# Kernel tuning notes

Hardware: AMD Instinct MI355X
Metric: run time of the kernel (lower is better)

## Reference

```python
import jax, jax.numpy as jnp
import numpy as np

# RVQECell configuration (matches init_kwargs)
I_SZ, W_SZ, STAGES, ORDER, DEGREE = 6, 12, 3, 2, 2
BIAS = float(np.pi / 2)
ANC = ORDER - 1                      # ancillas_for_order(order) = order - 1
N = I_SZ + W_SZ + ANC                # 19 qubits
B = 32
INOUT = list(range(I_SZ))            # lanes 0..5
WORK = list(range(I_SZ, I_SZ + W_SZ))  # lanes 6..17
C_CTRL = I_SZ + W_SZ - 1             # controls per neuron = 17


def setup_inputs() -> dict:
    key = jax.random.key(0)
    ks = jax.random.split(key, 9)
    s = 0.1  # small init keeps neuron angles in a well-conditioned range
    psi = jax.random.normal(ks[0], (B, 2 ** N), jnp.float32)
    psi = psi / jnp.linalg.norm(psi, axis=1, keepdims=True)  # normalized kets
    return {
        "batch": psi,
        "w_in1": jax.random.normal(ks[1], (W_SZ, C_CTRL), jnp.float32) * s,
        "w_in2": jax.random.normal(ks[2], (W_SZ, C_CTRL, C_CTRL), jnp.float32) * s,
        "w_u": jax.random.normal(ks[3], (STAGES, W_SZ), jnp.float32) * s,
        "w_k1": jax.random.normal(ks[4], (STAGES, W_SZ, C_CTRL), jnp.float32) * s,
        "w_k2": jax.random.normal(ks[5], (STAGES, W_SZ, C_CTRL, C_CTRL), jnp.float32) * s,
        "w_out1": jax.random.normal(ks[6], (I_SZ, C_CTRL), jnp.float32) * s,
        "w_out2": jax.random.normal(ks[7], (I_SZ, C_CTRL, C_CTRL), jnp.float32) * s,
        "inputs": jax.random.randint(ks[8], (B, I_SZ), 0, 2, dtype=jnp.int32),
    }


def _rot_y(state, lane, alpha):
    # real rotation [[cos a, -sin a], [sin a, cos a]] on qubit `lane`.
    ax = lane + 1  # +1 for batch axis; state shape [B] + [2]*N
    c, s = jnp.cos(alpha), jnp.sin(alpha)
    p0 = jax.lax.index_in_dim(state, 0, ax, keepdims=True)
    p1 = jax.lax.index_in_dim(state, 1, ax, keepdims=True)
    return jnp.concatenate([c * p0 - s * p1, s * p0 + c * p1], axis=ax)


def _neuron(state, outlane, th1, th2):
    # Fast (deterministic RUS) quantum neuron of given ORDER/DEGREE:
    # per control-basis-branch rotation of `outlane` by alpha(x),
    # phi(x) = bias + sum_i th1_i x_i + sum_{i<j} th2_ij x_i x_j (degree 2),
    # alpha = q^(order-1)(phi), q(t) = arctan(tan(t)^2), stable via arctan2.
    controls = [l for l in range(I_SZ + W_SZ) if l != outlane]
    Cn = len(controls)
    x = jnp.arange(2 ** Cn)
    shifts = jnp.arange(Cn - 1, -1, -1)
    bits = ((x[:, None] >> shifts[None, :]) & 1).astype(state.dtype)  # [2^Cn, Cn]
    phi = BIAS + bits @ th1
    if DEGREE >= 2:
        phi = phi + jnp.einsum('xi,ij,xj->x', bits, jnp.triu(th2, 1), bits)
    alpha = phi
    for _ in range(ORDER - 1):
        alpha = jnp.arctan2(jnp.sin(alpha) ** 2, jnp.cos(alpha) ** 2)
    shape = [1] + [2 if l in controls else 1 for l in range(N)]
    return _rot_y(state, outlane, alpha.reshape(shape))


def _bitflip(state_flat, inputs):
    # Vectorized batched BitFlipLayer: X on inout lane i where inputs[b,i]==1,
    # i.e. permute amplitudes by XOR of the flip mask (lane 0 most significant).
    shifts = (N - 1) - jnp.arange(I_SZ)
    f = jnp.sum(inputs.astype(jnp.int32) << shifts[None, :], axis=1)  # [B]
    idx = jnp.arange(2 ** N, dtype=jnp.int32)[None, :] ^ f[:, None]
    return jnp.take_along_axis(state_flat, idx, axis=1)


def reference(batch, w_in1, w_in2, w_u, w_k1, w_k2, w_out1, w_out2, inputs):
    psi = _bitflip(batch, inputs).reshape((B,) + (2,) * N)
    # input layer: one neuron per workspace lane
    for j, out in enumerate(WORK):
        psi = _neuron(psi, out, w_in1[j], w_in2[j])
    # kernel layer: stages x (UnitaryLayer(workspace) + neurons)
    for st in range(STAGES):
        for j, lane in enumerate(WORK):
            psi = _rot_y(psi, lane, w_u[st, j])
        for j, out in enumerate(WORK):
            psi = _neuron(psi, out, w_k1[st, j], w_k2[st, j])
    psi = _bitflip(psi.reshape(B, -1), inputs).reshape((B,) + (2,) * N)
    # output layer: one neuron per inout lane
    for j, out in enumerate(INOUT):
        psi = _neuron(psi, out, w_out1[j], w_out2[j])
    # measurement probabilities over inout lanes: marginal of |amp|^2
    probs = jnp.sum(psi ** 2, axis=tuple(range(1 + I_SZ, 1 + N))).reshape(B, -1)
    return probs, psi.reshape(B, -1)
```

## Files before the change

### kernel.cpp

```cpp
#include <hip/hip_runtime.h>
#include <math.h>


#define BIAS_F 1.57079632679489662f

typedef float v4f __attribute__((ext_vector_type(4)));

__device__ __forceinline__ float4 ntload4(const float* p) {
    v4f v = __builtin_nontemporal_load((const v4f*)p);
    return make_float4(v.x, v.y, v.z, v.w);
}
__device__ __forceinline__ void ntstore4(float* p, float4 f) {
    v4f v = {f.x, f.y, f.z, f.w};
    __builtin_nontemporal_store(v, (v4f*)p);
}

__device__ __forceinline__ int SW(int i) { return i ^ ((i >> 3) & 0x1C); }
__device__ __forceinline__ float4 ldsld4(const float* st, int i) {
    return *(const float4*)&st[SW(i)];
}
__device__ __forceinline__ void ldsst4(float* st, int i, float4 v) {
    *(float4*)&st[SW(i)] = v;
}

#define LD2(p) (*(const float2*)(p))
#define LD4(p) (*(const float4*)(p))

__device__ __forceinline__ void rot4(float4& A, float4& B, float4 e) {
    float ax = A.x, ay = A.y, az = A.z, aw = A.w;
    A.x = e.x * ax - e.y * B.x;  B.x = e.y * ax + e.x * B.x;
    A.y = e.x * ay - e.y * B.y;  B.y = e.y * ay + e.x * B.y;
    A.z = e.z * az - e.w * B.z;  B.z = e.w * az + e.z * B.z;
    A.w = e.z * aw - e.w * B.w;  B.w = e.w * aw + e.z * B.w;
}
__device__ __forceinline__ void rotq(float4& P, float c, float s) {
    float px = P.x, py = P.y;
    P.x = c * px - s * P.z;  P.z = s * px + c * P.z;
    P.y = c * py - s * P.w;  P.w = s * py + c * P.w;
}


__global__ __launch_bounds__(256) void tables_kernel(
    const float* __restrict__ w_in1, const float* __restrict__ w_in2,
    const float* __restrict__ w_k1,  const float* __restrict__ w_k2,
    const float* __restrict__ w_out1, const float* __restrict__ w_out2,
    float* __restrict__ tab)
{
    const int n = blockIdx.y;
    const int hi = blockIdx.x;
    const int tid = threadIdx.x;
    const float* th1;
    const float* th2;
    if (n < 12)      { th1 = w_in1 + n * 17;         th2 = w_in2 + n * 289; }
    else if (n < 48) { th1 = w_k1 + (n - 12) * 17;   th2 = w_k2 + (n - 12) * 289; }
    else             { th1 = w_out1 + (n - 48) * 17; th2 = w_out2 + (n - 48) * 289; }

    float phi_hi = BIAS_F;
    float C[8];
#pragma unroll
    for (int a = 0; a < 8; ++a) C[a] = th1[9 + a];
#pragma unroll
    for (int i = 0; i < 9; ++i) {
        if ((hi >> (8 - i)) & 1) {
            float acc = th1[i];
#pragma unroll
            for (int j = i + 1; j < 9; ++j)
                if ((hi >> (8 - j)) & 1) acc += th2[i * 17 + j];
            phi_hi += acc;
#pragma unroll
            for (int a = 0; a < 8; ++a) C[a] += th2[i * 17 + 9 + a];
        }
    }

    float bt[8];
#pragma unroll
    for (int j = 0; j < 8; ++j) bt[j] = (float)((tid >> (7 - j)) & 1);
    float phi = phi_hi;
#pragma unroll
    for (int a = 0; a < 8; ++a) {
        float acc = C[a];
#pragma unroll
        for (int b2 = a + 1; b2 < 8; ++b2) acc += bt[b2] * th2[(9 + a) * 17 + 9 + b2];
        phi += bt[a] * acc;
    }

    float sp, cp;
    sincosf(phi, &sp, &cp);
    float c2 = cp * cp, s2 = sp * sp;
    float d = c2 * c2 + s2 * s2;
    float r = rsqrtf(d);
    r = r * (1.5f - 0.5f * d * r * r);
    float2* dst = (float2*)tab + ((size_t)n * 131072 + (size_t)((hi << 8) | tid));
    *dst = make_float2(c2 * r, s2 * r);
}

template <int PA, bool NEUR>
__device__ __forceinline__ void pass_hi2(float* l0, float* l1, int t8,
    const float* tA, const float* tB, const float* tC,
    float cA, float sA, float cB, float sB, float cC, float sC)
{
    const int lowb = PA - 4;
    const int low = t8 & ((1 << lowb) - 1);
    const int high = t8 >> lowb;
    const int i0 = (high << (PA + 1)) | (low << 2);
    const int x0 = (high << (PA - 1)) | (low << 1);
    const int oa = 1 << PA, ob = oa >> 1, oc = oa >> 2;
    const int dhi = oa >> 2, dlo = oa >> 3;
    float4 ea00, ea01, ea10, ea11, eb00, eb01, eb10, eb11, ec00, ec01, ec10, ec11;
    if (NEUR) {
        ea00 = LD4(&tA[2 * x0]);            ea01 = LD4(&tA[2 * (x0 + dlo)]);
        ea10 = LD4(&tA[2 * (x0 + dhi)]);    ea11 = LD4(&tA[2 * (x0 + dhi + dlo)]);
        eb00 = LD4(&tB[2 * x0]);            eb01 = LD4(&tB[2 * (x0 + dlo)]);
        eb10 = LD4(&tB[2 * (x0 + dhi)]);    eb11 = LD4(&tB[2 * (x0 + dhi + dlo)]);
        ec00 = LD4(&tC[2 * x0]);            ec01 = LD4(&tC[2 * (x0 + dlo)]);
        ec10 = LD4(&tC[2 * (x0 + dhi)]);    ec11 = LD4(&tC[2 * (x0 + dhi + dlo)]);
    } else {
        ea00 = ea01 = ea10 = ea11 = make_float4(cA, sA, cA, sA);
        eb00 = eb01 = eb10 = eb11 = make_float4(cB, sB, cB, sB);
        ec00 = ec01 = ec10 = ec11 = make_float4(cC, sC, cC, sC);
    }
#pragma unroll
    for (int s = 0; s < 2; ++s) {
        float* sl = (s == 0) ? l0 : l1;
        float4 Q000 = ldsld4(sl, i0),            Q001 = ldsld4(sl, i0 + oc);
        float4 Q010 = ldsld4(sl, i0 + ob),       Q011 = ldsld4(sl, i0 + ob + oc);
        float4 Q100 = ldsld4(sl, i0 + oa),       Q101 = ldsld4(sl, i0 + oa + oc);
        float4 Q110 = ldsld4(sl, i0 + oa + ob),  Q111 = ldsld4(sl, i0 + oa + ob + oc);
        rot4(Q000, Q100, ea00); rot4(Q001, Q101, ea01);
        rot4(Q010, Q110, ea10); rot4(Q011, Q111, ea11);
        rot4(Q000, Q010, eb00); rot4(Q001, Q011, eb01);
        rot4(Q100, Q110, eb10); rot4(Q101, Q111, eb11);
        rot4(Q000, Q001, ec00); rot4(Q010, Q011, ec01);
        rot4(Q100, Q101, ec10); rot4(Q110, Q111, ec11);
        ldsst4(sl, i0, Q000);            ldsst4(sl, i0 + oc, Q001);
        ldsst4(sl, i0 + ob, Q010);       ldsst4(sl, i0 + ob + oc, Q011);
        ldsst4(sl, i0 + oa, Q100);       ldsst4(sl, i0 + oa + oc, Q101);
        ldsst4(sl, i0 + oa + ob, Q110);  ldsst4(sl, i0 + oa + ob + oc, Q111);
    }
}

template <bool NEUR>
__device__ __forceinline__ void pass_lo2(float* l0, float* l1, int t8,
    const float* tA, const float* tB, const float* tC,
    float cA, float sA, float cB, float sB, float cC, float sC)
{
    const int i0 = t8 << 5, x0 = t8 << 3;
    float4 ea0, ea1, ea2, ea3, eb0, eb1, eb2, eb3, ec0, ec1, ec2, ec3;
    if (NEUR) {
        ea0 = LD4(&tA[2 * x0]);      ea1 = LD4(&tA[2 * x0 + 4]);
        ea2 = LD4(&tA[2 * x0 + 8]);  ea3 = LD4(&tA[2 * x0 + 12]);
        eb0 = LD4(&tB[2 * x0]);      eb1 = LD4(&tB[2 * x0 + 4]);
        eb2 = LD4(&tB[2 * x0 + 8]);  eb3 = LD4(&tB[2 * x0 + 12]);
        ec0 = LD4(&tC[2 * x0]);      ec1 = LD4(&tC[2 * x0 + 4]);
        ec2 = LD4(&tC[2 * x0 + 8]);  ec3 = LD4(&tC[2 * x0 + 12]);
    } else {
        ea0 = ea1 = ea2 = ea3 = make_float4(cA, sA, cA, sA);
        eb0 = eb1 = eb2 = eb3 = make_float4(cB, sB, cB, sB);
        ec0 = ec1 = ec2 = ec3 = make_float4(cC, sC, cC, sC);
    }
#pragma unroll
    for (int s = 0; s < 2; ++s) {
        float* sl = (s == 0) ? l0 : l1;
        float4 Q0 = ldsld4(sl, i0),      Q1 = ldsld4(sl, i0 + 4);
        float4 Q2 = ldsld4(sl, i0 + 8),  Q3 = ldsld4(sl, i0 + 12);
        float4 Q4 = ldsld4(sl, i0 + 16), Q5 = ldsld4(sl, i0 + 20);
        float4 Q6 = ldsld4(sl, i0 + 24), Q7 = ldsld4(sl, i0 + 28);
        rot4(Q0, Q2, ea0); rot4(Q1, Q3, ea1); rot4(Q4, Q6, ea2); rot4(Q5, Q7, ea3);
        rot4(Q0, Q1, eb0); rot4(Q2, Q3, eb1); rot4(Q4, Q5, eb2); rot4(Q6, Q7, eb3);
        rotq(Q0, ec0.x, ec0.y); rotq(Q1, ec0.z, ec0.w);
        rotq(Q2, ec1.x, ec1.y); rotq(Q3, ec1.z, ec1.w);
        rotq(Q4, ec2.x, ec2.y); rotq(Q5, ec2.z, ec2.w);
        rotq(Q6, ec3.x, ec3.y); rotq(Q7, ec3.z, ec3.w);
        ldsst4(sl, i0, Q0);      ldsst4(sl, i0 + 4, Q1);
        ldsst4(sl, i0 + 8, Q2);  ldsst4(sl, i0 + 12, Q3);
        ldsst4(sl, i0 + 16, Q4); ldsst4(sl, i0 + 20, Q5);
        ldsst4(sl, i0 + 24, Q6); ldsst4(sl, i0 + 28, Q7);
    }
}

__global__ __launch_bounds__(256, 2) void main_kernel(
    const float* __restrict__ batch, const float* __restrict__ w_u,
    const int* __restrict__ inputs, const float* __restrict__ tab,
    float* __restrict__ psi, float* __restrict__ probs)
{
    __shared__ __align__(16) float lds[2][8192];
    const int t8 = threadIdx.x;
    const int blk = blockIdx.x;
    const int xcd = blk & 7;
    const int vt = (xcd << 3) | ((blk >> 3) & 7);
    const int pair = blk >> 6;

    if (blk == 0) {
        float4 z = make_float4(0.f, 0.f, 0.f, 0.f);
        *(float4*)&probs[t8 * 8] = z;
        *(float4*)&probs[t8 * 8 + 4] = z;
    }

    int bb[2], uu[2];
#pragma unroll
    for (int s = 0; s < 2; ++s) {
        int b = pair * 2 + s;
        int fb = 0;
#pragma unroll
        for (int i = 0; i < 6; ++i) fb |= (inputs[b * 6 + i] & 1) << (5 - i);
        bb[s] = b; uu[s] = vt ^ fb;
        const float* src = batch + ((size_t)b << 19) + ((size_t)uu[s] << 13);
#pragma unroll
        for (int k = 0; k < 8; ++k) {
            int i4 = (k * 256 + t8) * 4;
            float4 v = ntload4(&src[i4]);
            *(float4*)&lds[s][SW(i4)] = v;
        }
    }
    float* l0 = lds[0];
    float* l1 = lds[1];

    const float* tb = tab + ((size_t)vt << 12);
#define TN(j) (tb + (size_t)(j) * 262144)
#define BAR __syncthreads()
    BAR;
    pass_hi2<12, true>(l0, l1, t8, TN(0), TN(1), TN(2), 0,0,0,0,0,0);  BAR;
    pass_hi2<9,  true>(l0, l1, t8, TN(3), TN(4), TN(5), 0,0,0,0,0,0);  BAR;
    pass_hi2<6,  true>(l0, l1, t8, TN(6), TN(7), TN(8), 0,0,0,0,0,0);  BAR;
    pass_lo2<true>(l0, l1, t8, TN(9), TN(10), TN(11), 0,0,0,0,0,0);    BAR;

#pragma unroll 1
    for (int st2 = 0; st2 < 3; ++st2) {
        const float* wu = w_u + st2 * 12;
        float c0, s0, c1, s1, c2, s2;
        sincosf(wu[0], &s0, &c0); sincosf(wu[1], &s1, &c1); sincosf(wu[2], &s2, &c2);
        pass_hi2<12, false>(l0, l1, t8, 0,0,0, c0,s0, c1,s1, c2,s2);   BAR;
        sincosf(wu[3], &s0, &c0); sincosf(wu[4], &s1, &c1); sincosf(wu[5], &s2, &c2);
        pass_hi2<9, false>(l0, l1, t8, 0,0,0, c0,s0, c1,s1, c2,s2);    BAR;
        sincosf(wu[6], &s0, &c0); sincosf(wu[7], &s1, &c1); sincosf(wu[8], &s2, &c2);
        pass_hi2<6, false>(l0, l1, t8, 0,0,0, c0,s0, c1,s1, c2,s2);    BAR;
        sincosf(wu[9], &s0, &c0); sincosf(wu[10], &s1, &c1); sincosf(wu[11], &s2, &c2);
        pass_lo2<false>(l0, l1, t8, 0,0,0, c0,s0, c1,s1, c2,s2);       BAR;

        const int nb = 12 + st2 * 12;
        pass_hi2<12, true>(l0, l1, t8, TN(nb+0), TN(nb+1), TN(nb+2), 0,0,0,0,0,0); BAR;
        pass_hi2<9,  true>(l0, l1, t8, TN(nb+3), TN(nb+4), TN(nb+5), 0,0,0,0,0,0); BAR;
        pass_hi2<6,  true>(l0, l1, t8, TN(nb+6), TN(nb+7), TN(nb+8), 0,0,0,0,0,0); BAR;
        pass_lo2<true>(l0, l1, t8, TN(nb+9), TN(nb+10), TN(nb+11), 0,0,0,0,0,0);   BAR;
    }
#undef TN
#undef BAR

#pragma unroll
    for (int s = 0; s < 2; ++s) {
        float* dst = psi + ((size_t)bb[s] << 19) + ((size_t)uu[s] << 13);
#pragma unroll
        for (int k = 0; k < 8; ++k) {
            int i4 = (k * 256 + t8) * 4;
            float4 v = *(const float4*)&lds[s][SW(i4)];
            ntstore4(&dst[i4], v);
        }
    }
}

__global__ __launch_bounds__(256, 2) void out_kernel(
    const float* __restrict__ tab, float* __restrict__ psi,
    float* __restrict__ probs)
{
    __shared__ __align__(16) float ts[16384];
    const int tid = threadIdx.x;
    const int lane = tid & 63;
    const int wv = tid >> 6;
    const int b = blockIdx.x >> 5;
    const int c0 = (blockIdx.x & 31) << 8;
    float* gbase = psi + ((size_t)b << 19) + c0;

#pragma unroll
    for (int i = 0; i < 16; ++i) {
        int k = wv * 16 + i;
        float4 v = ntload4(&gbase[((size_t)k << 13) + lane * 4]);
        int f4 = lane ^ (k & 15);
        *(float4*)&ts[k * 256 + f4 * 4] = v;
    }
    __syncthreads();

    float a[64];
#pragma unroll
    for (int k = 0; k < 64; ++k) a[k] = ts[k * 256 + (tid ^ ((k & 15) << 2))];
    const int w12 = (c0 | tid) >> 1;

#define OSTAGE(J) { \
    const float* tj = tab + 2u * ((size_t)(48 + (J)) * 131072 + (size_t)w12); \
    _Pragma("unroll") \
    for (int h = 0; h < 2; ++h) { \
        float2 ev[16]; \
        _Pragma("unroll") \
        for (int m = 0; m < 16; ++m) ev[m] = LD2(&tj[(size_t)(h * 16 + m) << 13]); \
        _Pragma("unroll") \
        for (int m = 0; m < 16; ++m) { \
            const int mm = h * 16 + m; \
            const int q = 5 - (J); \
            const int k0 = ((mm >> q) << (q + 1)) | (mm & ((1 << q) - 1)); \
            const int k1 = k0 | (1 << q); \
            float2 e = ev[m]; \
            float A0 = a[k0], A1 = a[k1]; \
            a[k0] = e.x * A0 - e.y * A1; \
            a[k1] = e.y * A0 + e.x * A1; } } }
    OSTAGE(0) OSTAGE(1) OSTAGE(2) OSTAGE(3) OSTAGE(4) OSTAGE(5)
#undef OSTAGE

#pragma unroll
    for (int k = 0; k < 64; ++k) ts[k * 256 + (tid ^ ((k & 15) << 2))] = a[k];
    __syncthreads();

#pragma unroll
    for (int i = 0; i < 16; ++i) {
        int k = wv * 16 + i;
        int f4 = lane ^ (k & 15);
        float4 v = *(const float4*)&ts[k * 256 + f4 * 4];
        ntstore4(&gbase[((size_t)k << 13) + lane * 4], v);
    }

    const int k6 = tid & 63, seg = tid >> 6;
    float p = 0.f;
#pragma unroll
    for (int j = 0; j < 64; ++j) {
        int c = seg * 64 + ((j + k6) & 63);
        float v = ts[k6 * 256 + (c ^ ((k6 & 15) << 2))];
        p += v * v;
    }
    atomicAdd(&probs[b * 64 + k6], p);
}

extern "C" void kernel_launch(void* const* d_in, const int* in_sizes, int n_in,
                              void* d_out, int out_size, void* d_ws, size_t ws_size,
                              hipStream_t stream)
{
    const float* batch  = (const float*)d_in[0];
    const float* w_in1  = (const float*)d_in[1];
    const float* w_in2  = (const float*)d_in[2];
    const float* w_u    = (const float*)d_in[3];
    const float* w_k1   = (const float*)d_in[4];
    const float* w_k2   = (const float*)d_in[5];
    const float* w_out1 = (const float*)d_in[6];
    const float* w_out2 = (const float*)d_in[7];
    const int*   inputs = (const int*)d_in[8];
    float* probs = (float*)d_out;
    float* psi   = (float*)d_out + 2048;
    float* tab   = (float*)d_ws;

    tables_kernel<<<dim3(512, 54), 256, 0, stream>>>(w_in1, w_in2, w_k1, w_k2,
                                                     w_out1, w_out2, tab);
    main_kernel<<<1024, 256, 0, stream>>>(batch, w_u, inputs, tab, psi, probs);
    out_kernel<<<1024, 256, 0, stream>>>(tab, psi, probs);
}
```

Before: 328.3 us.

## Process one batch slice per block and fuse unitary pass into neuron pass

Each block now handles a single batch slice with half the LDS, so the grid doubles and occupancy is raised to 4 blocks per CU. Table values are loaded just before each rotation instead of all up front, which lowers register pressure. The unitary pass on lanes 12-bit is reordered and fused into the following neuron pass on the same qubits, removing one LDS round trip and one barrier per stage. In exchange, the neuron tables are reloaded once per batch slice instead of being shared across two slices.

Result: slower. 416.0 us (+26.7%).

```diff
diff --git a/kernel.cpp b/kernel.cpp
--- a/kernel.cpp
+++ b/kernel.cpp
@@ -94,8 +94,8 @@
     *dst = make_float2(c2 * r, s2 * r);
 }
 
-template <int PA, bool NEUR>
-__device__ __forceinline__ void pass_hi2(float* l0, float* l1, int t8,
+template <int PA, bool NEUR, bool UNI>
+__device__ __forceinline__ void pass_hi1(float* sl, int t8,
     const float* tA, const float* tB, const float* tC,
     float cA, float sA, float cB, float sB, float cC, float sC)
 {
@@ -106,89 +106,88 @@
     const int x0 = (high << (PA - 1)) | (low << 1);
     const int oa = 1 << PA, ob = oa >> 1, oc = oa >> 2;
     const int dhi = oa >> 2, dlo = oa >> 3;
-    float4 ea00, ea01, ea10, ea11, eb00, eb01, eb10, eb11, ec00, ec01, ec10, ec11;
+    float4 Q000 = ldsld4(sl, i0),            Q001 = ldsld4(sl, i0 + oc);
+    float4 Q010 = ldsld4(sl, i0 + ob),       Q011 = ldsld4(sl, i0 + ob + oc);
+    float4 Q100 = ldsld4(sl, i0 + oa),       Q101 = ldsld4(sl, i0 + oa + oc);
+    float4 Q110 = ldsld4(sl, i0 + oa + ob),  Q111 = ldsld4(sl, i0 + oa + ob + oc);
+    if (UNI || !NEUR) {
+        float4 eA = make_float4(cA, sA, cA, sA);
+        rot4(Q000, Q100, eA); rot4(Q001, Q101, eA);
+        rot4(Q010, Q110, eA); rot4(Q011, Q111, eA);
+        float4 eB = make_float4(cB, sB, cB, sB);
+        rot4(Q000, Q010, eB); rot4(Q001, Q011, eB);
+        rot4(Q100, Q110, eB); rot4(Q101, Q111, eB);
+        float4 eC = make_float4(cC, sC, cC, sC);
+        rot4(Q000, Q001, eC); rot4(Q010, Q011, eC);
+        rot4(Q100, Q101, eC); rot4(Q110, Q111, eC);
+    }
     if (NEUR) {
-        ea00 = LD4(&tA[2 * x0]);            ea01 = LD4(&tA[2 * (x0 + dlo)]);
-        ea10 = LD4(&tA[2 * (x0 + dhi)]);    ea11 = LD4(&tA[2 * (x0 + dhi + dlo)]);
-        eb00 = LD4(&tB[2 * x0]);            eb01 = LD4(&tB[2 * (x0 + dlo)]);
-        eb10 = LD4(&tB[2 * (x0 + dhi)]);    eb11 = LD4(&tB[2 * (x0 + dhi + dlo)]);
-        ec00 = LD4(&tC[2 * x0]);            ec01 = LD4(&tC[2 * (x0 + dlo)]);
-        ec10 = LD4(&tC[2 * (x0 + dhi)]);    ec11 = LD4(&tC[2 * (x0 + dhi + dlo)]);
-    } else {
-        ea00 = ea01 = ea10 = ea11 = make_float4(cA, sA, cA, sA);
-        eb00 = eb01 = eb10 = eb11 = make_float4(cB, sB, cB, sB);
-        ec00 = ec01 = ec10 = ec11 = make_float4(cC, sC, cC, sC);
-    }
-#pragma unroll
-    for (int s = 0; s < 2; ++s) {
-        float* sl = (s == 0) ? l0 : l1;
-        float4 Q000 = ldsld4(sl, i0),            Q001 = ldsld4(sl, i0 + oc);
-        float4 Q010 = ldsld4(sl, i0 + ob),       Q011 = ldsld4(sl, i0 + ob + oc);
-        float4 Q100 = ldsld4(sl, i0 + oa),       Q101 = ldsld4(sl, i0 + oa + oc);
-        float4 Q110 = ldsld4(sl, i0 + oa + ob),  Q111 = ldsld4(sl, i0 + oa + ob + oc);
-        rot4(Q000, Q100, ea00); rot4(Q001, Q101, ea01);
-        rot4(Q010, Q110, ea10); rot4(Q011, Q111, ea11);
-        rot4(Q000, Q010, eb00); rot4(Q001, Q011, eb01);
-        rot4(Q100, Q110, eb10); rot4(Q101, Q111, eb11);
-        rot4(Q000, Q001, ec00); rot4(Q010, Q011, ec01);
-        rot4(Q100, Q101, ec10); rot4(Q110, Q111, ec11);
-        ldsst4(sl, i0, Q000);            ldsst4(sl, i0 + oc, Q001);
-        ldsst4(sl, i0 + ob, Q010);       ldsst4(sl, i0 + ob + oc, Q011);
-        ldsst4(sl, i0 + oa, Q100);       ldsst4(sl, i0 + oa + oc, Q101);
-        ldsst4(sl, i0 + oa + ob, Q110);  ldsst4(sl, i0 + oa + ob + oc, Q111);
-    }
+        float4 e0 = LD4(&tA[2 * x0]),            e1 = LD4(&tA[2 * (x0 + dlo)]);
+        float4 e2 = LD4(&tA[2 * (x0 + dhi)]),    e3 = LD4(&tA[2 * (x0 + dhi + dlo)]);
+        rot4(Q000, Q100, e0); rot4(Q001, Q101, e1);
+        rot4(Q010, Q110, e2); rot4(Q011, Q111, e3);
+        e0 = LD4(&tB[2 * x0]);          e1 = LD4(&tB[2 * (x0 + dlo)]);
+        e2 = LD4(&tB[2 * (x0 + dhi)]);  e3 = LD4(&tB[2 * (x0 + dhi + dlo)]);
+        rot4(Q000, Q010, e0); rot4(Q001, Q011, e1);
+        rot4(Q100, Q110, e2); rot4(Q101, Q111, e3);
+        e0 = LD4(&tC[2 * x0]);          e1 = LD4(&tC[2 * (x0 + dlo)]);
+        e2 = LD4(&tC[2 * (x0 + dhi)]);  e3 = LD4(&tC[2 * (x0 + dhi + dlo)]);
+        rot4(Q000, Q001, e0); rot4(Q010, Q011, e1);
+        rot4(Q100, Q101, e2); rot4(Q110, Q111, e3);
+    }
+    ldsst4(sl, i0, Q000);            ldsst4(sl, i0 + oc, Q001);
+    ldsst4(sl, i0 + ob, Q010);       ldsst4(sl, i0 + ob + oc, Q011);
+    ldsst4(sl, i0 + oa, Q100);       ldsst4(sl, i0 + oa + oc, Q101);
+    ldsst4(sl, i0 + oa + ob, Q110);  ldsst4(sl, i0 + oa + ob + oc, Q111);
 }
 
 template <bool NEUR>
-__device__ __forceinline__ void pass_lo2(float* l0, float* l1, int t8,
+__device__ __forceinline__ void pass_lo1(float* sl, int t8,
     const float* tA, const float* tB, const float* tC,
     float cA, float sA, float cB, float sB, float cC, float sC)
 {
     const int i0 = t8 << 5, x0 = t8 << 3;
-    float4 ea0, ea1, ea2, ea3, eb0, eb1, eb2, eb3, ec0, ec1, ec2, ec3;
+    float4 Q0 = ldsld4(sl, i0),      Q1 = ldsld4(sl, i0 + 4);
+    float4 Q2 = ldsld4(sl, i0 + 8),  Q3 = ldsld4(sl, i0 + 12);
+    float4 Q4 = ldsld4(sl, i0 + 16), Q5 = ldsld4(sl, i0 + 20);
+    float4 Q6 = ldsld4(sl, i0 + 24), Q7 = ldsld4(sl, i0 + 28);
     if (NEUR) {
-        ea0 = LD4(&tA[2 * x0]);      ea1 = LD4(&tA[2 * x0 + 4]);
-        ea2 = LD4(&tA[2 * x0 + 8]);  ea3 = LD4(&tA[2 * x0 + 12]);
-        eb0 = LD4(&tB[2 * x0]);      eb1 = LD4(&tB[2 * x0 + 4]);
-        eb2 = LD4(&tB[2 * x0 + 8]);  eb3 = LD4(&tB[2 * x0 + 12]);
-        ec0 = LD4(&tC[2 * x0]);      ec1 = LD4(&tC[2 * x0 + 4]);
-        ec2 = LD4(&tC[2 * x0 + 8]);  ec3 = LD4(&tC[2 * x0 + 12]);
+        float4 e0 = LD4(&tA[2 * x0]),     e1 = LD4(&tA[2 * x0 + 4]);
+        float4 e2 = LD4(&tA[2 * x0 + 8]), e3 = LD4(&tA[2 * x0 + 12]);
+        rot4(Q0, Q2, e0); rot4(Q1, Q3, e1); rot4(Q4, Q6, e2); rot4(Q5, Q7, e3);
+        e0 = LD4(&tB[2 * x0]);     e1 = LD4(&tB[2 * x0 + 4]);
+        e2 = LD4(&tB[2 * x0 + 8]); e3 = LD4(&tB[2 * x0 + 12]);
+        rot4(Q0, Q1, e0); rot4(Q2, Q3, e1); rot4(Q4, Q5, e2); rot4(Q6, Q7, e3);
+        e0 = LD4(&tC[2 * x0]);     e1 = LD4(&tC[2 * x0 + 4]);
+        e2 = LD4(&tC[2 * x0 + 8]); e3 = LD4(&tC[2 * x0 + 12]);
+        rotq(Q0, e0.x, e0.y); rotq(Q1, e0.z, e0.w);
+        rotq(Q2, e1.x, e1.y); rotq(Q3, e1.z, e1.w);
+        rotq(Q4, e2.x, e2.y); rotq(Q5, e2.z, e2.w);
+        rotq(Q6, e3.x, e3.y); rotq(Q7, e3.z, e3.w);
     } else {
-        ea0 = ea1 = ea2 = ea3 = make_float4(cA, sA, cA, sA);
-        eb0 = eb1 = eb2 = eb3 = make_float4(cB, sB, cB, sB);
-        ec0 = ec1 = ec2 = ec3 = make_float4(cC, sC, cC, sC);
-    }
-#pragma unroll
-    for (int s = 0; s < 2; ++s) {
-        float* sl = (s == 0) ? l0 : l1;
-        float4 Q0 = ldsld4(sl, i0),      Q1 = ldsld4(sl, i0 + 4);
-        float4 Q2 = ldsld4(sl, i0 + 8),  Q3 = ldsld4(sl, i0 + 12);
-        float4 Q4 = ldsld4(sl, i0 + 16), Q5 = ldsld4(sl, i0 + 20);
-        float4 Q6 = ldsld4(sl, i0 + 24), Q7 = ldsld4(sl, i0 + 28);
-        rot4(Q0, Q2, ea0); rot4(Q1, Q3, ea1); rot4(Q4, Q6, ea2); rot4(Q5, Q7, ea3);
-        rot4(Q0, Q1, eb0); rot4(Q2, Q3, eb1); rot4(Q4, Q5, eb2); rot4(Q6, Q7, eb3);
-        rotq(Q0, ec0.x, ec0.y); rotq(Q1, ec0.z, ec0.w);
-        rotq(Q2, ec1.x, ec1.y); rotq(Q3, ec1.z, ec1.w);
-        rotq(Q4, ec2.x, ec2.y); rotq(Q5, ec2.z, ec2.w);
-        rotq(Q6, ec3.x, ec3.y); rotq(Q7, ec3.z, ec3.w);
-        ldsst4(sl, i0, Q0);      ldsst4(sl, i0 + 4, Q1);
-        ldsst4(sl, i0 + 8, Q2);  ldsst4(sl, i0 + 12, Q3);
-        ldsst4(sl, i0 + 16, Q4); ldsst4(sl, i0 + 20, Q5);
-        ldsst4(sl, i0 + 24, Q6); ldsst4(sl, i0 + 28, Q7);
-    }
-}
-
-__global__ __launch_bounds__(256, 2) void main_kernel(
+        float4 eA = make_float4(cA, sA, cA, sA);
+        rot4(Q0, Q2, eA); rot4(Q1, Q3, eA); rot4(Q4, Q6, eA); rot4(Q5, Q7, eA);
+        float4 eB = make_float4(cB, sB, cB, sB);
+        rot4(Q0, Q1, eB); rot4(Q2, Q3, eB); rot4(Q4, Q5, eB); rot4(Q6, Q7, eB);
+        rotq(Q0, cC, sC); rotq(Q1, cC, sC); rotq(Q2, cC, sC); rotq(Q3, cC, sC);
+        rotq(Q4, cC, sC); rotq(Q5, cC, sC); rotq(Q6, cC, sC); rotq(Q7, cC, sC);
+    }
+    ldsst4(sl, i0, Q0);      ldsst4(sl, i0 + 4, Q1);
+    ldsst4(sl, i0 + 8, Q2);  ldsst4(sl, i0 + 12, Q3);
+    ldsst4(sl, i0 + 16, Q4); ldsst4(sl, i0 + 20, Q5);
+    ldsst4(sl, i0 + 24, Q6); ldsst4(sl, i0 + 28, Q7);
+}
+
+__global__ __launch_bounds__(256, 4) void main_kernel(
     const float* __restrict__ batch, const float* __restrict__ w_u,
     const int* __restrict__ inputs, const float* __restrict__ tab,
     float* __restrict__ psi, float* __restrict__ probs)
 {
-    __shared__ __align__(16) float lds[2][8192];
+    __shared__ __align__(16) float sl[8192];
     const int t8 = threadIdx.x;
     const int blk = blockIdx.x;
-    const int xcd = blk & 7;
-    const int vt = (xcd << 3) | ((blk >> 3) & 7);
-    const int pair = blk >> 6;
+    const int vt = blk & 63;
+    const int b = blk >> 6;
 
     if (blk == 0) {
         float4 z = make_float4(0.f, 0.f, 0.f, 0.f);
@@ -196,63 +195,58 @@
         *(float4*)&probs[t8 * 8 + 4] = z;
     }
 
-    int bb[2], uu[2];
-#pragma unroll
-    for (int s = 0; s < 2; ++s) {
-        int b = pair * 2 + s;
-        int fb = 0;
-#pragma unroll
-        for (int i = 0; i < 6; ++i) fb |= (inputs[b * 6 + i] & 1) << (5 - i);
-        bb[s] = b; uu[s] = vt ^ fb;
-        const float* src = batch + ((size_t)b << 19) + ((size_t)uu[s] << 13);
+    int fb = 0;
+#pragma unroll
+    for (int i = 0; i < 6; ++i) fb |= (inputs[b * 6 + i] & 1) << (5 - i);
+    const int u = vt ^ fb;
+    {
+        const float* src = batch + ((size_t)b << 19) + ((size_t)u << 13);
 #pragma unroll
         for (int k = 0; k < 8; ++k) {
             int i4 = (k * 256 + t8) * 4;
             float4 v = ntload4(&src[i4]);
-            *(float4*)&lds[s][SW(i4)] = v;
+            *(float4*)&sl[SW(i4)] = v;
         }
     }
-    float* l0 = lds[0];
-    float* l1 = lds[1];
 
     const float* tb = tab + ((size_t)vt << 12);
 #define TN(j) (tb + (size_t)(j) * 262144)
 #define BAR __syncthreads()
     BAR;
-    pass_hi2<12, true>(l0, l1, t8, TN(0), TN(1), TN(2), 0,0,0,0,0,0);  BAR;
-    pass_hi2<9,  true>(l0, l1, t8, TN(3), TN(4), TN(5), 0,0,0,0,0,0);  BAR;
-    pass_hi2<6,  true>(l0, l1, t8, TN(6), TN(7), TN(8), 0,0,0,0,0,0);  BAR;
-    pass_lo2<true>(l0, l1, t8, TN(9), TN(10), TN(11), 0,0,0,0,0,0);    BAR;
+    pass_hi1<12, true, false>(sl, t8, TN(0), TN(1), TN(2), 0,0,0,0,0,0);  BAR;
+    pass_hi1<9,  true, false>(sl, t8, TN(3), TN(4), TN(5), 0,0,0,0,0,0);  BAR;
+    pass_hi1<6,  true, false>(sl, t8, TN(6), TN(7), TN(8), 0,0,0,0,0,0);  BAR;
+    pass_lo1<true>(sl, t8, TN(9), TN(10), TN(11), 0,0,0,0,0,0);           BAR;
 
 #pragma unroll 1
     for (int st2 = 0; st2 < 3; ++st2) {
         const float* wu = w_u + st2 * 12;
+        const int nb = 12 + st2 * 12;
         float c0, s0, c1, s1, c2, s2;
+
+        sincosf(wu[3], &s0, &c0); sincosf(wu[4], &s1, &c1); sincosf(wu[5], &s2, &c2);
+        pass_hi1<9, false, false>(sl, t8, 0,0,0, c0,s0, c1,s1, c2,s2);    BAR;
+        sincosf(wu[6], &s0, &c0); sincosf(wu[7], &s1, &c1); sincosf(wu[8], &s2, &c2);
+        pass_hi1<6, false, false>(sl, t8, 0,0,0, c0,s0, c1,s1, c2,s2);    BAR;
+        sincosf(wu[9], &s0, &c0); sincosf(wu[10], &s1, &c1); sincosf(wu[11], &s2, &c2);
+        pass_lo1<false>(sl, t8, 0,0,0, c0,s0, c1,s1, c2,s2);              BAR;
+
         sincosf(wu[0], &s0, &c0); sincosf(wu[1], &s1, &c1); sincosf(wu[2], &s2, &c2);
-        pass_hi2<12, false>(l0, l1, t8, 0,0,0, c0,s0, c1,s1, c2,s2);   BAR;
-        sincosf(wu[3], &s0, &c0); sincosf(wu[4], &s1, &c1); sincosf(wu[5], &s2, &c2);
-        pass_hi2<9, false>(l0, l1, t8, 0,0,0, c0,s0, c1,s1, c2,s2);    BAR;
-        sincosf(wu[6], &s0, &c0); sincosf(wu[7], &s1, &c1); sincosf(wu[8], &s2, &c2);
-        pass_hi2<6, false>(l0, l1, t8, 0,0,0, c0,s0, c1,s1, c2,s2);    BAR;
-        sincosf(wu[9], &s0, &c0); sincosf(wu[10], &s1, &c1); sincosf(wu[11], &s2, &c2);
-        pass_lo2<false>(l0, l1, t8, 0,0,0, c0,s0, c1,s1, c2,s2);       BAR;
-
-        const int nb = 12 + st2 * 12;
-        pass_hi2<12, true>(l0, l1, t8, TN(nb+0), TN(nb+1), TN(nb+2), 0,0,0,0,0,0); BAR;
-        pass_hi2<9,  true>(l0, l1, t8, TN(nb+3), TN(nb+4), TN(nb+5), 0,0,0,0,0,0); BAR;
-        pass_hi2<6,  true>(l0, l1, t8, TN(nb+6), TN(nb+7), TN(nb+8), 0,0,0,0,0,0); BAR;
-        pass_lo2<true>(l0, l1, t8, TN(nb+9), TN(nb+10), TN(nb+11), 0,0,0,0,0,0);   BAR;
+        pass_hi1<12, true, true>(sl, t8, TN(nb+0), TN(nb+1), TN(nb+2),
+                                 c0,s0, c1,s1, c2,s2);                    BAR;
+        pass_hi1<9,  true, false>(sl, t8, TN(nb+3), TN(nb+4), TN(nb+5), 0,0,0,0,0,0); BAR;
+        pass_hi1<6,  true, false>(sl, t8, TN(nb+6), TN(nb+7), TN(nb+8), 0,0,0,0,0,0); BAR;
+        pass_lo1<true>(sl, t8, TN(nb+9), TN(nb+10), TN(nb+11), 0,0,0,0,0,0);          BAR;
     }
 #undef TN
 #undef BAR
 
-#pragma unroll
-    for (int s = 0; s < 2; ++s) {
-        float* dst = psi + ((size_t)bb[s] << 19) + ((size_t)uu[s] << 13);
+    {
+        float* dst = psi + ((size_t)b << 19) + ((size_t)u << 13);
 #pragma unroll
         for (int k = 0; k < 8; ++k) {
             int i4 = (k * 256 + t8) * 4;
-            float4 v = *(const float4*)&lds[s][SW(i4)];
+            float4 v = *(const float4*)&sl[SW(i4)];
             ntstore4(&dst[i4], v);
         }
     }
@@ -346,6 +340,6 @@
 
     tables_kernel<<<dim3(512, 54), 256, 0, stream>>>(w_in1, w_in2, w_k1, w_k2,
                                                      w_out1, w_out2, tab);
-    main_kernel<<<1024, 256, 0, stream>>>(batch, w_u, inputs, tab, psi, probs);
+    main_kernel<<<2048, 256, 0, stream>>>(batch, w_u, inputs, tab, psi, probs);
     out_kernel<<<1024, 256, 0, stream>>>(tab, psi, probs);
 }
```
